# Kernel tuning notes

Hardware: AMD Instinct MI355X
Metric: run time of the kernel (lower is better)

Reference implementation:

```python
import jax, jax.numpy as jnp
import numpy as np

DIM = 256
NUM_HEADS = 8


def setup_inputs() -> dict:
    key = jax.random.key(0)
    ks = jax.random.split(key, 5)
    x = jax.random.normal(ks[0], (32, DIM, 56, 56), dtype=jnp.float32)
    # Conv2d(dim, 2*dim, k=1, groups=2): weight [2*dim, dim//2, 1, 1]
    qk_w = jax.random.normal(ks[1], (2 * DIM, DIM // 2, 1, 1), dtype=jnp.float32) * (DIM // 2) ** -0.5
    qk_b = jax.random.normal(ks[2], (2 * DIM,), dtype=jnp.float32) * 0.02
    # Conv2d(dim, dim, k=3, pad=1, groups=dim): weight [dim, 1, 3, 3]
    pe_w = jax.random.normal(ks[3], (DIM, 1, 3, 3), dtype=jnp.float32) * (1.0 / 3.0)
    pe_b = jax.random.normal(ks[4], (DIM,), dtype=jnp.float32) * 0.02
    return {"x": x, "qk_w": qk_w, "qk_b": qk_b, "pe_w": pe_w, "pe_b": pe_b}


def _conv(x, w, padding, groups):
    return jax.lax.conv_general_dilated(
        x, w, window_strides=(1, 1), padding=padding,
        feature_group_count=groups,
        dimension_numbers=("NCHW", "OIHW", "NCHW"))


def reference(x, qk_w, qk_b, pe_w, pe_b):
    b, c, h, w = x.shape
    H, hd = NUM_HEADS, c // NUM_HEADS
    n = h * w
    s = n ** (-0.5)

    # grouped 1x1 conv -> elu + 1 feature map
    qk = _conv(x, qk_w, "VALID", groups=2) + qk_b[None, :, None, None]
    qk = jax.nn.elu(qk) + 1.0                       # [b, 2c, h, w]
    qk = qk.reshape(b, 2, H, hd, n)
    q, k = qk[:, 0], qk[:, 1]                       # [b, H, hd, n]
    v = x.reshape(b, H, hd, n)                      # [b, H, hd, n]

    # kv = (k*s) @ (v^T * s)  -> [b, H, hd, hd]
    kv = jnp.einsum("bhdn,bhen->bhde", k * s, v * s)
    # numerator: q^T @ kv -> [b, H, n, hd]
    num = jnp.einsum("bhdn,bhde->bhne", q, kv)
    # denominator: q^T @ mean_n(k) -> [b, H, n]
    den = jnp.einsum("bhdn,bhd->bhn", q, k.mean(axis=-1))
    out = num / (den[..., None] + 1e-6)             # [b, H, n, hd]

    out = out.transpose(0, 1, 3, 2).reshape(b, c, h, w)
    pe = _conv(x, pe_w, [(1, 1), (1, 1)], groups=c) + pe_b[None, :, None, None]
    return out + pe
```

## Files before the change

### kernel.cpp

```cpp
#include <hip/hip_runtime.h>
#include <cmath>

#define NCH   256
#define NPIX  3136
#define NB    32
#define SEV   7
#define INV_N (1.0f / 3136.0f)

typedef __attribute__((ext_vector_type(8)))  short bf16x8;
typedef __attribute__((ext_vector_type(4)))  float f32x4;
typedef __attribute__((ext_vector_type(16))) float f32x16;

#define KV7_F  (SEV * NB * 8 * 1024)
#define KM7_F  (SEV * NB * 256)
#define KVF_F  (NB * 8 * 1024)
#define KMF_F  (NB * 256)
#define KM7_OFF (KV7_F)
#define KVF_OFF (KM7_OFF + KM7_F)
#define KMF_OFF (KVF_OFF + KVF_F)
#define WF_OFF  (KMF_OFF + KMF_F)

__device__ __forceinline__ ushort f2bf(float f) {
  unsigned u = __float_as_uint(f);
  u += 0x7FFFu + ((u >> 16) & 1u);
  return (ushort)(u >> 16);
}
__device__ __forceinline__ float bf2f(ushort h) {
  return __uint_as_float(((unsigned)h) << 16);
}

__global__ void wfrag_kernel(const float* __restrict__ qk_w, ushort* __restrict__ Wf) {
  const int tid = blockIdx.x * 512 + threadIdx.x;
  const int lane = tid & 63;
  const int ks = (tid >> 6) & 3;
  const int mt = (tid >> 8) & 15;
  const int hl = (tid >> 12) & 1;
  const int side = (tid >> 13) & 1;
  const int ch = mt * 16 + (lane & 15);
  const int oc = side * 256 + ch;
  ushort v[8];
#pragma unroll
  for (int j = 0; j < 8; ++j) {
    const int k = ks * 32 + (lane >> 4) * 8 + j;
    const float w = qk_w[(size_t)oc * 128 + k];
    const ushort hi = f2bf(w);
    v[j] = (hl == 0) ? hi : f2bf(w - bf2f(hi));
  }
  *(uint4*)(Wf + (size_t)tid * 8) = *(const uint4*)v;
}

__global__ __launch_bounds__(512, 4)
void kv_kernel(const float* __restrict__ x, const ushort* __restrict__ Wf,
               const float* __restrict__ qk_b, float* __restrict__ kv7,
               float* __restrict__ km7) {
  const int bid = blockIdx.x;
  const int hd = (bid >= 224) ? 1 : 0;
  const int rem = bid - hd * 224;
  const int sev = rem >> 5, b = rem & 31;
  const int t = threadIdx.x;
  const int w = t >> 6, l = t & 63;
  const int q = l >> 4, r15 = l & 15;
  const int e = l & 31, q5 = l >> 5;
  const int h_l = w & 3, ph = w >> 2;
  const int mt = w;

  __shared__ __align__(16) ushort Xb[64][152];
  __shared__ __align__(16) ushort KVs[2 * 128 * 88];
  ushort (*Kst)[88] = (ushort(*)[88])KVs;
  ushort (*Vst)[88] = (ushort(*)[88])(KVs + 128 * 88);

  bf16x8 wf[4][2];
#pragma unroll
  for (int ks = 0; ks < 4; ++ks)
#pragma unroll
    for (int hl = 0; hl < 2; ++hl) {
      const size_t off =
          (size_t)(((((2 + hl) * 16 + (hd * 8 + mt)) * 4 + ks) * 64 + l)) * 8;
      wf[ks][hl] = *(const bf16x8*)(Wf + off);
    }

  float bias[4];
#pragma unroll
  for (int r = 0; r < 4; ++r)
    bias[r] = qk_b[256 + hd * 128 + mt * 16 + q * 4 + r];

  f32x16 kvacc;
#pragma unroll
  for (int i = 0; i < 16; ++i) kvacc[i] = 0.f;
  float kmacc[4] = {0.f, 0.f, 0.f, 0.f};

  const float* xk = x + ((size_t)(b * NCH) + 128) * NPIX + sev * 448;
  const float* xv = x + ((size_t)(b * NCH)) * NPIX + sev * 448;

  for (int st = 0; st < SEV; ++st) {
    const int p0 = st * 64;
    __syncthreads();

#pragma unroll
    for (int rr = 0; rr < 4; ++rr) {
      const int id = t + 512 * rr;
      const int cc = id >> 4;
      const int pf = id & 15;
      const float4 v = *(const float4*)(xk + (size_t)cc * NPIX + p0 + pf * 4);
      const ushort b0 = f2bf(v.x), b1 = f2bf(v.y), b2 = f2bf(v.z), b3 = f2bf(v.w);
      Xb[pf * 4 + 0][cc] = b0;
      Xb[pf * 4 + 1][cc] = b1;
      Xb[pf * 4 + 2][cc] = b2;
      Xb[pf * 4 + 3][cc] = b3;
      if (hd == 1) {
        const uint2 pk = {(uint)b0 | ((uint)b1 << 16), (uint)b2 | ((uint)b3 << 16)};
        *(uint2*)&Vst[cc][pf * 4] = pk;
      }
    }
    if (hd == 0) {
#pragma unroll
      for (int rr = 0; rr < 4; ++rr) {
        const int id = t + 512 * rr;
        const int cc = id >> 4;
        const int pf = id & 15;
        const float4 v = *(const float4*)(xv + (size_t)cc * NPIX + p0 + pf * 4);
        const uint2 pk = {(uint)f2bf(v.x) | ((uint)f2bf(v.y) << 16),
                          (uint)f2bf(v.z) | ((uint)f2bf(v.w) << 16)};
        *(uint2*)&Vst[cc][pf * 4] = pk;
      }
    }
    __syncthreads();

    f32x4 acc[4];
#pragma unroll
    for (int nt = 0; nt < 4; ++nt)
#pragma unroll
      for (int r = 0; r < 4; ++r) acc[nt][r] = 0.f;
#pragma unroll
    for (int ks = 0; ks < 4; ++ks) {
      bf16x8 xbf[4];
#pragma unroll
      for (int nt = 0; nt < 4; ++nt)
        xbf[nt] = *(const bf16x8*)&Xb[nt * 16 + r15][ks * 32 + q * 8];
#pragma unroll
      for (int nt = 0; nt < 4; ++nt) {
        acc[nt] = __builtin_amdgcn_mfma_f32_16x16x32_bf16(wf[ks][0], xbf[nt], acc[nt], 0, 0, 0);
        acc[nt] = __builtin_amdgcn_mfma_f32_16x16x32_bf16(wf[ks][1], xbf[nt], acc[nt], 0, 0, 0);
      }
    }

#pragma unroll
    for (int nt = 0; nt < 4; ++nt) {
#pragma unroll
      for (int r = 0; r < 4; ++r) {
        float v = acc[nt][r] + bias[r];
        v = (v > 0.f) ? (v + 1.f) : __expf(v);
        kmacc[r] += v;
        Kst[mt * 16 + q * 4 + r][nt * 16 + r15] = f2bf(v);
      }
    }
    __syncthreads();

#pragma unroll
    for (int ks2 = 0; ks2 < 2; ++ks2) {
      const int kp = ph * 32 + ks2 * 16 + q5 * 8;
      const bf16x8 ak = *(const bf16x8*)&Kst[h_l * 32 + e][kp];
      const bf16x8 bv = *(const bf16x8*)&Vst[h_l * 32 + e][kp];
      kvacc = __builtin_amdgcn_mfma_f32_32x32x16_bf16(ak, bv, kvacc, 0, 0, 0);
    }
  }

  __syncthreads();
  float* red = (float*)KVs;
#pragma unroll
  for (int reg = 0; reg < 16; ++reg) {
    const int row = (reg & 3) + 8 * (reg >> 2) + 4 * q5;
    red[w * 1024 + row * 32 + e] = kvacc[reg];
  }
  __syncthreads();
#pragma unroll
  for (int i = 0; i < 8; ++i) {
    const int idx = t + 512 * i;
    const int hl2 = idx >> 10;
    const int el = idx & 1023;
    const float s = red[hl2 * 1024 + el] + red[(hl2 + 4) * 1024 + el];
    kv7[(((size_t)sev * NB + b) * 8 + hd * 4 + hl2) * 1024 + el] = s;
  }
#pragma unroll
  for (int r = 0; r < 4; ++r) {
    float s = kmacc[r];
    s += __shfl_xor(s, 1);
    s += __shfl_xor(s, 2);
    s += __shfl_xor(s, 4);
    s += __shfl_xor(s, 8);
    if (r15 == 0)
      km7[((size_t)sev * NB + b) * 256 + hd * 128 + mt * 16 + q * 4 + r] = s;
  }
}

__global__ void red_kernel(const float* __restrict__ kv7, const float* __restrict__ km7,
                           float* __restrict__ kvF, float* __restrict__ kmF) {
  const int b = blockIdx.x;
  const int t = threadIdx.x;
  for (int i = t; i < 8192; i += 256) {
    float s = 0.f;
#pragma unroll
    for (int sv = 0; sv < SEV; ++sv)
      s += kv7[(size_t)(sv * NB + b) * 8192 + i];
    kvF[(size_t)b * 8192 + i] = s * INV_N;
  }
  {
    float s = 0.f;
#pragma unroll
    for (int sv = 0; sv < SEV; ++sv)
      s += km7[(size_t)(sv * NB + b) * 256 + t];
    kmF[b * 256 + t] = s * INV_N;
  }
}

__global__ __launch_bounds__(512, 4)
void out_kernel(const float* __restrict__ x, const ushort* __restrict__ Wf,
                const float* __restrict__ qk_b, const float* __restrict__ kvF,
                const float* __restrict__ kmF, float* __restrict__ out) {
  const int bid = blockIdx.x;
  const int hd = (bid >= 224) ? 1 : 0;
  const int rem = bid - hd * 224;
  const int b = rem & 31, sev = rem >> 5;
  const int t = threadIdx.x;
  const int w = t >> 6, l = t & 63;
  const int q = l >> 4, r15 = l & 15;
  const int mt = w;
  const int h_l = w & 3, eh = w >> 2;

  __shared__ ushort Xb[64][136];
  __shared__ ushort QT[64][136];
  __shared__ float denP[8][64];

  bf16x8 wf[4][2];
#pragma unroll
  for (int ks = 0; ks < 4; ++ks)
#pragma unroll
    for (int hl = 0; hl < 2; ++hl) {
      const size_t off =
          (size_t)((((hl * 16 + (hd * 8 + mt)) * 4 + ks) * 64 + l)) * 8;
      wf[ks][hl] = *(const bf16x8*)(Wf + off);
    }

  float bias[4], kmw[4];
#pragma unroll
  for (int r = 0; r < 4; ++r) {
    const int c = hd * 128 + mt * 16 + q * 4 + r;
    bias[r] = qk_b[c];
    kmw[r] = kmF[b * 256 + c];
  }

  bf16x8 bkv;
  {
    const int hg = hd * 4 + h_l;
#pragma unroll
    for (int j = 0; j < 8; ++j)
      bkv[j] = (short)f2bf(
          kvF[(size_t)b * 8192 + hg * 1024 + (q * 8 + j) * 32 + eh * 16 + r15]);
  }

  const float* xq = x + (size_t)(b * NCH) * NPIX + sev * 448;

  for (int st = 0; st < SEV; ++st) {
    const int pos0 = st * 64;
#pragma unroll
    for (int rr = 0; rr < 4; ++rr) {
      const int id = t + 512 * rr;
      const int ch = id >> 4;
      const int p4 = (id & 15) * 4;
      const float4 v = *(const float4*)(xq + (size_t)ch * NPIX + pos0 + p4);
      Xb[p4 + 0][ch] = f2bf(v.x);
      Xb[p4 + 1][ch] = f2bf(v.y);
      Xb[p4 + 2][ch] = f2bf(v.z);
      Xb[p4 + 3][ch] = f2bf(v.w);
    }
    __syncthreads();

    f32x4 acc[4];
#pragma unroll
    for (int nt = 0; nt < 4; ++nt)
#pragma unroll
      for (int r = 0; r < 4; ++r) acc[nt][r] = 0.f;
#pragma unroll
    for (int ks = 0; ks < 4; ++ks) {
      bf16x8 xbf[4];
#pragma unroll
      for (int nt = 0; nt < 4; ++nt)
        xbf[nt] = *(const bf16x8*)&Xb[nt * 16 + r15][ks * 32 + q * 8];
#pragma unroll
      for (int nt = 0; nt < 4; ++nt) {
        acc[nt] = __builtin_amdgcn_mfma_f32_16x16x32_bf16(wf[ks][0], xbf[nt], acc[nt], 0, 0, 0);
        acc[nt] = __builtin_amdgcn_mfma_f32_16x16x32_bf16(wf[ks][1], xbf[nt], acc[nt], 0, 0, 0);
      }
    }

#pragma unroll
    for (int nt = 0; nt < 4; ++nt) {
      ushort pk[4];
      float dsum = 0.f;
#pragma unroll
      for (int r = 0; r < 4; ++r) {
        float v = acc[nt][r] + bias[r];
        v = (v > 0.f) ? (v + 1.f) : __expf(v);
        pk[r] = f2bf(v);
        dsum += v * kmw[r];
      }
      *(uint2*)&QT[nt * 16 + r15][mt * 16 + q * 4] = *(const uint2*)pk;
      dsum += __shfl_xor(dsum, 16);
      dsum += __shfl_xor(dsum, 32);
      if (q == 0) denP[mt][nt * 16 + r15] = dsum;
    }
    __syncthreads();

#pragma unroll
    for (int pt = 0; pt < 4; ++pt) {
      const bf16x8 aq = *(const bf16x8*)&QT[pt * 16 + r15][h_l * 32 + q * 8];
      f32x4 z;
      z[0] = z[1] = z[2] = z[3] = 0.f;
      const f32x4 n0 = __builtin_amdgcn_mfma_f32_16x16x32_bf16(aq, bkv, z, 0, 0, 0);
      float4 o0;
      float rdn[4];
#pragma unroll
      for (int r = 0; r < 4; ++r) {
        const int pl = pt * 16 + q * 4 + r;
        rdn[r] = 1.0f / (denP[2 * h_l][pl] + denP[2 * h_l + 1][pl] + 1e-6f);
      }
      o0.x = n0[0] * rdn[0]; o0.y = n0[1] * rdn[1];
      o0.z = n0[2] * rdn[2]; o0.w = n0[3] * rdn[3];
      const int posg = sev * 448 + pos0 + pt * 16 + q * 4;
      const int c = hd * 128 + h_l * 32 + eh * 16 + r15;
      *(float4*)(out + ((size_t)(b * NCH + c)) * NPIX + posg) = o0;
    }
  }
}

__global__ __launch_bounds__(512, 4)
void pe_kernel(const float* __restrict__ x, const float* __restrict__ pe_w,
               const float* __restrict__ pe_b, float* __restrict__ out) {
  const int b = blockIdx.y;
  const int c0 = blockIdx.x * 4;
  const int t = threadIdx.x;
  const int wave = t >> 6;
  const int cl = wave & 3;
  const int rh = wave >> 2;
  const int lane = t & 63;

  __shared__ float xs[4][NPIX];

#pragma unroll
  for (int cc = 0; cc < 4; ++cc) {
    const float4* src = (const float4*)(x + ((size_t)(b * NCH + c0 + cc)) * NPIX);
    float4* dst = (float4*)&xs[cc][0];
    for (int i = t; i < NPIX / 4; i += 512) dst[i] = src[i];
  }
  __syncthreads();

  const int c = c0 + cl;
  float pw[9];
#pragma unroll
  for (int i = 0; i < 9; ++i) pw[i] = pe_w[c * 9 + i];
  const float pb = pe_b[c];
  float* oc = out + ((size_t)(b * NCH + c)) * NPIX;
  const float* xc = xs[cl];

  if (lane < 56) {
    const bool hasL = (lane > 0), hasR = (lane < 55);
    for (int rg = 0; rg < 7; ++rg) {
      const int rbase = rh * 28 + rg * 4;
      float o[4];
#pragma unroll
      for (int k = 0; k < 4; ++k) o[k] = oc[(rbase + k) * 56 + lane];
#pragma unroll
      for (int k = 0; k < 4; ++k) {
        const int r = rbase + k;
        float s = pb;
#pragma unroll
        for (int dy = -1; dy <= 1; ++dy) {
          const int rr = r + dy;
          if (rr < 0 || rr >= 56) continue;
          const float* xrow = xc + rr * 56 + lane;
          if (hasL) s += pw[(dy + 1) * 3 + 0] * xrow[-1];
          s += pw[(dy + 1) * 3 + 1] * xrow[0];
          if (hasR) s += pw[(dy + 1) * 3 + 2] * xrow[1];
        }
        o[k] += s;
      }
#pragma unroll
      for (int k = 0; k < 4; ++k) oc[(rbase + k) * 56 + lane] = o[k];
    }
  }
}

extern "C" void kernel_launch(void* const* d_in, const int* in_sizes, int n_in,
                              void* d_out, int out_size, void* d_ws,
                              size_t ws_size, hipStream_t stream) {
  const float* x    = (const float*)d_in[0];
  const float* qk_w = (const float*)d_in[1];
  const float* qk_b = (const float*)d_in[2];
  const float* pe_w = (const float*)d_in[3];
  const float* pe_b = (const float*)d_in[4];
  float* out = (float*)d_out;

  float* wsf = (float*)d_ws;
  float* kv7 = wsf;
  float* km7 = wsf + KM7_OFF;
  float* kvF = wsf + KVF_OFF;
  float* kmF = wsf + KMF_OFF;
  ushort* Wf = (ushort*)(wsf + WF_OFF);

  wfrag_kernel<<<32, 512, 0, stream>>>(qk_w, Wf);
  kv_kernel<<<448, 512, 0, stream>>>(x, Wf, qk_b, kv7, km7);
  red_kernel<<<NB, 256, 0, stream>>>(kv7, km7, kvF, kmF);
  out_kernel<<<448, 512, 0, stream>>>(x, Wf, qk_b, kvF, kmF, out);

  dim3 g3(64, NB);
  pe_kernel<<<g3, 512, 0, stream>>>(x, pe_w, pe_b, out);
}
```

Baseline: 151.2 us.

## Fuse depthwise 3x3 positional conv into out_kernel epilogue

```diff
diff --git a/kernel.cpp b/kernel.cpp
--- a/kernel.cpp
+++ b/kernel.cpp
@@ -216,7 +216,8 @@
 __global__ __launch_bounds__(512, 4)
 void out_kernel(const float* __restrict__ x, const ushort* __restrict__ Wf,
                 const float* __restrict__ qk_b, const float* __restrict__ kvF,
-                const float* __restrict__ kmF, float* __restrict__ out) {
+                const float* __restrict__ kmF, const float* __restrict__ pe_w,
+                const float* __restrict__ pe_b, float* __restrict__ out) {
   const int bid = blockIdx.x;
   const int hd = (bid >= 224) ? 1 : 0;
   const int rem = bid - hd * 224;
@@ -330,62 +331,47 @@
       const int c = hd * 128 + h_l * 32 + eh * 16 + r15;
       *(float4*)(out + ((size_t)(b * NCH + c)) * NPIX + posg) = o0;
     }
-  }
-}
-
-__global__ __launch_bounds__(512, 4)
-void pe_kernel(const float* __restrict__ x, const float* __restrict__ pe_w,
-               const float* __restrict__ pe_b, float* __restrict__ out) {
-  const int b = blockIdx.y;
-  const int c0 = blockIdx.x * 4;
-  const int t = threadIdx.x;
-  const int wave = t >> 6;
-  const int cl = wave & 3;
-  const int rh = wave >> 2;
-  const int lane = t & 63;
-
-  __shared__ float xs[4][NPIX];
-
-#pragma unroll
-  for (int cc = 0; cc < 4; ++cc) {
-    const float4* src = (const float4*)(x + ((size_t)(b * NCH + c0 + cc)) * NPIX);
-    float4* dst = (float4*)&xs[cc][0];
-    for (int i = t; i < NPIX / 4; i += 512) dst[i] = src[i];
-  }
+    __syncthreads();
+  }
+
   __syncthreads();
 
-  const int c = c0 + cl;
-  float pw[9];
-#pragma unroll
-  for (int i = 0; i < 9; ++i) pw[i] = pe_w[c * 9 + i];
-  const float pb = pe_b[c];
-  float* oc = out + ((size_t)(b * NCH + c)) * NPIX;
-  const float* xc = xs[cl];
-
-  if (lane < 56) {
-    const bool hasL = (lane > 0), hasR = (lane < 55);
-    for (int rg = 0; rg < 7; ++rg) {
-      const int rbase = rh * 28 + rg * 4;
-      float o[4];
-#pragma unroll
-      for (int k = 0; k < 4; ++k) o[k] = oc[(rbase + k) * 56 + lane];
-#pragma unroll
-      for (int k = 0; k < 4; ++k) {
-        const int r = rbase + k;
-        float s = pb;
-#pragma unroll
-        for (int dy = -1; dy <= 1; ++dy) {
-          const int rr = r + dy;
-          if (rr < 0 || rr >= 56) continue;
-          const float* xrow = xc + rr * 56 + lane;
-          if (hasL) s += pw[(dy + 1) * 3 + 0] * xrow[-1];
-          s += pw[(dy + 1) * 3 + 1] * xrow[0];
-          if (hasR) s += pw[(dy + 1) * 3 + 2] * xrow[1];
-        }
-        o[k] += s;
-      }
-#pragma unroll
-      for (int k = 0; k < 4; ++k) oc[(rbase + k) * 56 + lane] = o[k];
+  const bool act = (l < 56);
+  const int colv = act ? l : 55;
+  const bool hasL = act && (l > 0);
+  const bool hasR = (l < 55);
+  const int lnL = (l + 63) & 63, lnR = (l + 1) & 63;
+  const int gr0 = sev * 8;
+
+  for (int ci = 0; ci < 16; ++ci) {
+    const int c = hd * 128 + w * 16 + ci;
+    const float* xc = x + ((size_t)(b * NCH + c)) * NPIX;
+    float* ocp = out + ((size_t)(b * NCH + c)) * NPIX;
+    float pw[9];
+#pragma unroll
+    for (int i = 0; i < 9; ++i) pw[i] = pe_w[c * 9 + i];
+    const float pb = pe_b[c];
+
+    float mC = (gr0 > 0) ? xc[(gr0 - 1) * 56 + colv] : 0.f;
+    float cC = xc[gr0 * 56 + colv];
+    float mL = __shfl(mC, lnL), mR = __shfl(mC, lnR);
+    float cL = __shfl(cC, lnL), cR = __shfl(cC, lnR);
+
+#pragma unroll
+    for (int r = 0; r < 8; ++r) {
+      const int grp = gr0 + r + 1;
+      const float pCv = (grp < 56) ? xc[grp * 56 + colv] : 0.f;
+      const float pL = __shfl(pCv, lnL);
+      const float pR = __shfl(pCv, lnR);
+      float s = pb + pw[1] * mC + pw[4] * cC + pw[7] * pCv;
+      if (hasL) s += pw[0] * mL + pw[3] * cL + pw[6] * pL;
+      if (hasR) s += pw[2] * mR + pw[5] * cR + pw[8] * pR;
+      if (act) {
+        float* op = ocp + (gr0 + r) * 56 + l;
+        *op += s;
+      }
+      mC = cC; mL = cL; mR = cR;
+      cC = pCv; cL = pL; cR = pR;
     }
   }
 }
@@ -410,8 +396,5 @@
   wfrag_kernel<<<32, 512, 0, stream>>>(qk_w, Wf);
   kv_kernel<<<448, 512, 0, stream>>>(x, Wf, qk_b, kv7, km7);
   red_kernel<<<NB, 256, 0, stream>>>(kv7, km7, kvF, kmF);
-  out_kernel<<<448, 512, 0, stream>>>(x, Wf, qk_b, kvF, kmF, out);
-
-  dim3 g3(64, NB);
-  pe_kernel<<<g3, 512, 0, stream>>>(x, pe_w, pe_b, out);
-}
+  out_kernel<<<448, 512, 0, stream>>>(x, Wf, qk_b, kvF, kmF, pe_w, pe_b, out);
+}
```

Measured after the change: 182.5 us. 1.21x slower.
